# Optimization experiments

Hardware: AMD Instinct MI355X
Metric: run time of the kernel (lower is better)

The kernel has to match this reference:

```python
import jax, jax.numpy as jnp
import numpy as np

GAMMA = 2.5
K = 4
RHO = 0.085
TAU_CLIP = 5.0
NUM_HEADS = 8


def setup_inputs() -> dict:
    key = jax.random.key(0)
    ks = jax.random.split(key, 4)
    B, T, C = 2, 2048, 512
    x = jax.random.normal(ks[0], (B, T, C), jnp.float32)
    tau = jax.random.uniform(ks[1], (B, T, T), jnp.float32)
    s = 1.0 / np.sqrt(C)
    Wqkv = jax.random.normal(ks[2], (C, 3 * C), jnp.float32) * s
    bqkv = jnp.zeros((3 * C,), jnp.float32)
    Wproj = jax.random.normal(ks[3], (C, C), jnp.float32) * s
    bproj = jnp.zeros((C,), jnp.float32)
    return dict(x=x, tau=tau, Wqkv=Wqkv, bqkv=bqkv, Wproj=Wproj, bproj=bproj)


def reference(x, tau, Wqkv, bqkv, Wproj, bproj):
    B, T, C = x.shape
    H = NUM_HEADS
    D = C // H
    qkv = x @ Wqkv + bqkv                       # [B,T,3C]
    q, k, v = jnp.split(qkv, 3, axis=-1)
    q = q.reshape(B, T, H, D).transpose(0, 2, 1, 3)   # [B,H,T,D]
    k = k.reshape(B, T, H, D).transpose(0, 2, 1, 3)
    v = v.reshape(B, T, H, D).transpose(0, 2, 1, 3)
    scale = D ** -0.5
    logits = jnp.einsum('bhtd,bhsd->bhts', q, k) * scale   # [B,H,T,T]
    pheromone_bias = GAMMA * jnp.log(tau + 1e-8)           # [B,T,T]
    logits = logits + pheromone_bias[:, None]
    # top-K keys per query from tau define the sparse mask (LOCAL_WINDOW=0)
    k_val = min(K, T)
    idx = jax.lax.top_k(tau, k_val)[1]                     # [B,T,K]
    mask = jnp.zeros((B, T, T), bool).at[
        jnp.arange(B)[:, None, None], jnp.arange(T)[None, :, None], idx
    ].set(True)
    logits = jnp.where(mask[:, None], logits, -jnp.inf)
    attn = jax.nn.softmax(logits, axis=-1)                 # [B,H,T,T]
    # EMA pheromone (tau) update, no gradient in original (torch.no_grad)
    signal = attn.mean(axis=1)                             # [B,T,T]
    tau_new = (1.0 - RHO) * tau + signal ** 3
    tau_new = tau_new / (tau_new.sum(axis=-1, keepdims=True) + 1e-8)
    tau_new = jnp.minimum(tau_new, TAU_CLIP)
    tau_new = jax.lax.stop_gradient(tau_new)
    out = jnp.einsum('bhts,bhsd->bthd', attn, v).reshape(B, T, C)
    out = out @ Wproj + bproj
    return out, tau_new
```

## Files before the change

### kernel.cpp

```cpp
#include <hip/hip_runtime.h>
#include <hip/hip_bf16.h>
#include <math.h>

#define BB 2
#define TT 2048
#define CC 512
#define HH 8
#define DD 64
#define KK 4
#define C3 1536
#define MROWS (BB*TT)

#define G1_NT (C3/64)
#define G1_BLOCKS (G1_NT*(MROWS/128))
#define G2_NT (CC/64)
#define G2_BLOCKS (G2_NT*(MROWS/128))

typedef __attribute__((ext_vector_type(8))) short bf16x8;
typedef __attribute__((ext_vector_type(4))) float floatx4;

static __device__ __forceinline__ unsigned short f2bf(float f) {
  unsigned int u = __float_as_uint(f);
  return (unsigned short)((u + 0x7fffu + ((u >> 16) & 1u)) >> 16);
}
static __device__ __forceinline__ float bf2f(unsigned short u) {
  return __uint_as_float(((unsigned int)u) << 16);
}

template<bool BF16OUT>
static __device__ __forceinline__ void gemm_body(
    int bid, int nt,
    const unsigned short* __restrict__ A,
    const unsigned short* __restrict__ Bt,
    const float* __restrict__ bias,
    void* __restrict__ Cout, int N, int K) {
  __shared__ bf16x8 As[128 * 4];
  __shared__ bf16x8 Bs[64 * 4];
  const int tid  = threadIdx.x;
  const int wave = tid >> 6;
  const int lane = tid & 63;
  const int n0 = (bid % nt) * 64;
  const int m0 = (bid / nt) * 128;
  const int m_off = (wave >> 1) * 64;
  const int n_off = (wave & 1) * 32;
  const int lrow = lane >> 2;
  const int lx   = ((lane & 3) ^ ((lane >> 3) & 3)) * 8;
  const int fr = lane & 15;
  const int fq = lane >> 4;
  const int key = (fr >> 1) & 3;

  floatx4 acc[4][2];
#pragma unroll
  for (int i = 0; i < 4; ++i)
#pragma unroll
    for (int j = 0; j < 2; ++j) acc[i][j] = (floatx4){0.f, 0.f, 0.f, 0.f};

  for (int k0 = 0; k0 < K; k0 += 32) {
#pragma unroll
    for (int s = 0; s < 2; ++s) {
      int q = wave * 2 + s;
      const unsigned short* ga = A + (size_t)(m0 + q * 16 + lrow) * K + k0 + lx;
      __builtin_amdgcn_global_load_lds(
          (const __attribute__((address_space(1))) void*)ga,
          (__attribute__((address_space(3))) void*)((char*)As + q * 1024), 16, 0, 0);
    }
    const unsigned short* gb = Bt + (size_t)(n0 + wave * 16 + lrow) * K + k0 + lx;
    __builtin_amdgcn_global_load_lds(
        (const __attribute__((address_space(1))) void*)gb,
        (__attribute__((address_space(3))) void*)((char*)Bs + wave * 1024), 16, 0, 0);
    __syncthreads();
    bf16x8 a[4], b[2];
#pragma unroll
    for (int i = 0; i < 4; ++i)
      a[i] = As[(m_off + i * 16 + fr) * 4 + (fq ^ key)];
#pragma unroll
    for (int j = 0; j < 2; ++j)
      b[j] = Bs[(n_off + j * 16 + fr) * 4 + (fq ^ key)];
#pragma unroll
    for (int i = 0; i < 4; ++i)
#pragma unroll
      for (int j = 0; j < 2; ++j)
        acc[i][j] = __builtin_amdgcn_mfma_f32_16x16x32_bf16(a[i], b[j], acc[i][j], 0, 0, 0);
    __syncthreads();
  }
#pragma unroll
  for (int j = 0; j < 2; ++j) {
    int col = n0 + n_off + j * 16 + fr;
    float bv = bias[col];
#pragma unroll
    for (int i = 0; i < 4; ++i) {
#pragma unroll
      for (int r = 0; r < 4; ++r) {
        int row = m0 + m_off + i * 16 + fq * 4 + r;
        float v = acc[i][j][r] + bv;
        if (BF16OUT) ((unsigned short*)Cout)[(size_t)row * N + col] = f2bf(v);
        else         ((float*)Cout)[(size_t)row * N + col] = v;
      }
    }
  }
}

static __device__ __forceinline__ bool kv_better(float av, int ai, float bv, int bi) {
  return av > bv || (av == bv && ai < bi);
}
static __device__ __forceinline__ void kv_ce(float* v, int* i, int a, int b) {
  if (!kv_better(v[a], i[a], v[b], i[b])) {
    float tv = v[a]; v[a] = v[b]; v[b] = tv;
    int   ti = i[a]; i[a] = i[b]; i[b] = ti;
  }
}
static __device__ __forceinline__ void kv_merge(
    float* av, int* ai, const float* bv, const int* bi) {
  float cv[4]; int ci[4];
#pragma unroll
  for (int j = 0; j < 4; ++j) {
    bool t = kv_better(av[j], ai[j], bv[3 - j], bi[3 - j]);
    cv[j] = t ? av[j] : bv[3 - j];
    ci[j] = t ? ai[j] : bi[3 - j];
  }
  kv_ce(cv, ci, 0, 2); kv_ce(cv, ci, 1, 3);
  kv_ce(cv, ci, 0, 1); kv_ce(cv, ci, 2, 3);
#pragma unroll
  for (int j = 0; j < 4; ++j) { av[j] = cv[j]; ai[j] = ci[j]; }
}

static __device__ __forceinline__ void transpose_body(
    int t, int nbx, const float* __restrict__ W, unsigned short* __restrict__ Wt,
    int R, int Cn) {
  __shared__ unsigned short tile[32][33];
  const int c0 = (t % nbx) * 32, r0 = (t / nbx) * 32;
  const int tx = threadIdx.x & 31, ty = threadIdx.x >> 5;
#pragma unroll
  for (int i = 0; i < 4; ++i) {
    int r = ty + i * 8;
    tile[r][tx] = f2bf(W[(size_t)(r0 + r) * Cn + c0 + tx]);
  }
  __syncthreads();
#pragma unroll
  for (int i = 0; i < 4; ++i) {
    int r = ty + i * 8;
    Wt[(size_t)(c0 + r) * R + r0 + tx] = tile[tx][r];
  }
}

__global__ __launch_bounds__(256) void prep_kernel(
    const float* __restrict__ x, unsigned short* __restrict__ x_bf,
    const float* __restrict__ Wqkv, unsigned short* __restrict__ wqkv_t,
    const float* __restrict__ Wproj, unsigned short* __restrict__ wproj_t) {
  const int bid = blockIdx.x;
  if (bid < 1024) {
    int g = bid * 256 + threadIdx.x;
    const float4* p = (const float4*)x;
    float4 f0 = p[g * 2], f1 = p[g * 2 + 1];
    union { unsigned short u[8]; uint4 v; } pk;
    pk.u[0]=f2bf(f0.x); pk.u[1]=f2bf(f0.y); pk.u[2]=f2bf(f0.z); pk.u[3]=f2bf(f0.w);
    pk.u[4]=f2bf(f1.x); pk.u[5]=f2bf(f1.y); pk.u[6]=f2bf(f1.z); pk.u[7]=f2bf(f1.w);
    ((uint4*)x_bf)[g] = pk.v;
  } else if (bid < 1024 + 768) {
    transpose_body(bid - 1024, C3 / 32, Wqkv, wqkv_t, CC, C3);
  } else {
    transpose_body(bid - 1792, CC / 32, Wproj, wproj_t, CC, CC);
  }
}

__global__ __launch_bounds__(256) void gemm1_kernel(
    const unsigned short* __restrict__ x_bf,
    const unsigned short* __restrict__ wqkv_t,
    const float* __restrict__ bqkv, unsigned short* __restrict__ qkv_bf) {
  gemm_body<true>(blockIdx.x, G1_NT, x_bf, wqkv_t, bqkv, qkv_bf, C3, CC);
}

__global__ __launch_bounds__(256) void row_kernel(
    const unsigned short* __restrict__ qkv, const float* __restrict__ tau,
    unsigned short* __restrict__ attn_bf, float* __restrict__ tau_out) {
  const int row  = blockIdx.x;
  const int b    = row >> 11;
  const int tid  = threadIdx.x;
  const int wv   = tid >> 6;
  const int lane = tid & 63;

  __shared__ int   idx4[KK];
  __shared__ float tau4[KK];
  __shared__ float ps[HH][KK];
  __shared__ float s3s[KK];
  __shared__ float swv[4][4];
  __shared__ int   swi[4][4];
  __shared__ float wsum[4];
  __shared__ float tot;

  const float4* rp = (const float4*)(tau + (size_t)row * TT);
  float4 f0 = rp[tid * 2], f1 = rp[tid * 2 + 1];
  float e[8] = { f0.x, f0.y, f0.z, f0.w, f1.x, f1.y, f1.z, f1.w };
  const int base = tid * 8;

  float tv[4] = { -1e30f, -1e30f, -1e30f, -1e30f };
  int   ti[4] = { 1 << 30, 1 << 30, 1 << 30, 1 << 30 };
#pragma unroll
  for (int k = 0; k < 8; ++k) {
    float v = e[k];
    if (v > tv[3]) {
      tv[3] = v; ti[3] = base + k;
      if (tv[3] > tv[2]) { float a=tv[2]; tv[2]=tv[3]; tv[3]=a; int c=ti[2]; ti[2]=ti[3]; ti[3]=c; }
      if (tv[2] > tv[1]) { float a=tv[1]; tv[1]=tv[2]; tv[2]=a; int c=ti[1]; ti[1]=ti[2]; ti[2]=c; }
      if (tv[1] > tv[0]) { float a=tv[0]; tv[0]=tv[1]; tv[1]=a; int c=ti[0]; ti[0]=ti[1]; ti[1]=c; }
    }
  }
#pragma unroll
  for (int step = 1; step <= 32; step <<= 1) {
    float bv[4]; int bi[4];
#pragma unroll
    for (int j = 0; j < 4; ++j) {
      bv[j] = __shfl_xor(tv[j], step, 64);
      bi[j] = __shfl_xor(ti[j], step, 64);
    }
    kv_merge(tv, ti, bv, bi);
  }
  if (lane == 0) {
#pragma unroll
    for (int j = 0; j < 4; ++j) { swv[wv][j] = tv[j]; swi[wv][j] = ti[j]; }
  }
  __syncthreads();
  if (tid == 0) {
    float m0[4], m1[4]; int x0[4], x1[4];
#pragma unroll
    for (int j = 0; j < 4; ++j) { m0[j] = swv[0][j]; x0[j] = swi[0][j]; }
#pragma unroll
    for (int j = 0; j < 4; ++j) { m1[j] = swv[1][j]; x1[j] = swi[1][j]; }
    kv_merge(m0, x0, m1, x1);
#pragma unroll
    for (int j = 0; j < 4; ++j) { m1[j] = swv[2][j]; x1[j] = swi[2][j]; }
    float m2[4]; int x2[4];
#pragma unroll
    for (int j = 0; j < 4; ++j) { m2[j] = swv[3][j]; x2[j] = swi[3][j]; }
    kv_merge(m1, x1, m2, x2);
    kv_merge(m0, x0, m1, x1);
#pragma unroll
    for (int j = 0; j < 4; ++j) { idx4[j] = x0[j]; tau4[j] = m0[j]; }
  }
  __syncthreads();

  int   i4[KK]; float t4[KK];
#pragma unroll
  for (int j = 0; j < KK; ++j) { i4[j] = idx4[j]; t4[j] = tau4[j]; }

#pragma unroll
  for (int hh = 0; hh < 2; ++hh) {
    const int h = wv + hh * 4;
    const float q = bf2f(qkv[(size_t)row * C3 + h * DD + lane]);
    float kv[KK], vv[KK];
#pragma unroll
    for (int j = 0; j < KK; ++j) {
      size_t bs = ((size_t)(b * TT + i4[j])) * C3 + h * DD + lane;
      kv[j] = bf2f(qkv[bs + CC]);
      vv[j] = bf2f(qkv[bs + 2 * CC]);
    }
    float p[KK];
#pragma unroll
    for (int j = 0; j < KK; ++j) p[j] = q * kv[j];
#pragma unroll
    for (int off = 32; off > 0; off >>= 1)
#pragma unroll
      for (int j = 0; j < KK; ++j) p[j] += __shfl_xor(p[j], off, 64);
    float logit[KK];
#pragma unroll
    for (int j = 0; j < KK; ++j)
      logit[j] = p[j] * 0.125f + 2.5f * logf(t4[j] + 1e-8f);
    float m = fmaxf(fmaxf(logit[0], logit[1]), fmaxf(logit[2], logit[3]));
    float den = 0.f;
#pragma unroll
    for (int j = 0; j < KK; ++j) { p[j] = expf(logit[j] - m); den += p[j]; }
    float inv = 1.f / den;
#pragma unroll
    for (int j = 0; j < KK; ++j) p[j] *= inv;
    float o = 0.f;
#pragma unroll
    for (int j = 0; j < KK; ++j) o += p[j] * vv[j];
    attn_bf[(size_t)row * CC + h * DD + lane] = f2bf(o);
    if (lane < KK) ps[h][lane] = p[lane];
  }
  __syncthreads();
  if (tid < KK) {
    float s = 0.f;
#pragma unroll
    for (int k = 0; k < HH; ++k) s += ps[k][tid];
    s *= (1.0f / HH);
    s3s[tid] = s * s * s;
  }
  __syncthreads();

  float s3[KK];
#pragma unroll
  for (int j = 0; j < KK; ++j) s3[j] = s3s[j];
  const float keep = 1.0f - 0.085f;
  float local = 0.f;
#pragma unroll
  for (int i = 0; i < 8; ++i) {
    float t = keep * e[i];
#pragma unroll
    for (int j = 0; j < KK; ++j)
      if (base + i == i4[j]) t += s3[j];
    e[i] = t;
    local += t;
  }
#pragma unroll
  for (int off = 32; off > 0; off >>= 1) local += __shfl_xor(local, off, 64);
  if (lane == 0) wsum[wv] = local;
  __syncthreads();
  if (tid == 0) tot = wsum[0] + wsum[1] + wsum[2] + wsum[3];
  __syncthreads();
  float inv = 1.f / (tot + 1e-8f);
  float4* op = (float4*)(tau_out + (size_t)row * TT);
  float4 o0 = { fminf(e[0]*inv,5.f), fminf(e[1]*inv,5.f), fminf(e[2]*inv,5.f), fminf(e[3]*inv,5.f) };
  float4 o1 = { fminf(e[4]*inv,5.f), fminf(e[5]*inv,5.f), fminf(e[6]*inv,5.f), fminf(e[7]*inv,5.f) };
  op[tid * 2] = o0;
  op[tid * 2 + 1] = o1;
}

__global__ __launch_bounds__(256) void gemm2_kernel(
    const unsigned short* __restrict__ attn_bf,
    const unsigned short* __restrict__ wproj_t,
    const float* __restrict__ bproj, float* __restrict__ out) {
  gemm_body<false>(blockIdx.x, G2_NT, attn_bf, wproj_t, bproj, out, CC, CC);
}

extern "C" void kernel_launch(void* const* d_in, const int* in_sizes, int n_in,
                              void* d_out, int out_size, void* d_ws, size_t ws_size,
                              hipStream_t stream) {
  const float* x     = (const float*)d_in[0];
  const float* tau   = (const float*)d_in[1];
  const float* Wqkv  = (const float*)d_in[2];
  const float* bqkv  = (const float*)d_in[3];
  const float* Wproj = (const float*)d_in[4];
  const float* bproj = (const float*)d_in[5];

  float* out     = (float*)d_out;
  float* tau_new = out + (size_t)MROWS * CC;

  char* w = (char*)d_ws;
  unsigned short* qkv_bf  = (unsigned short*)w; w += (size_t)MROWS * C3 * 2;
  unsigned short* x_bf    = (unsigned short*)w; w += (size_t)MROWS * CC * 2;
  unsigned short* wqkv_t  = (unsigned short*)w; w += (size_t)C3 * CC * 2;
  unsigned short* wproj_t = (unsigned short*)w; w += (size_t)CC * CC * 2;
  unsigned short* attn_bf = (unsigned short*)w;

  prep_kernel<<<2048, 256, 0, stream>>>(x, x_bf, Wqkv, wqkv_t, Wproj, wproj_t);

  gemm1_kernel<<<G1_BLOCKS, 256, 0, stream>>>(x_bf, wqkv_t, bqkv, qkv_bf);

  row_kernel<<<MROWS, 256, 0, stream>>>(qkv_bf, tau, attn_bf, tau_new);

  gemm2_kernel<<<G2_BLOCKS, 256, 0, stream>>>(attn_bf, wproj_t, bproj, out);
}
```

Measured before the change: 146.5 us.

## Add XCD-aware block swizzle, smaller gemm2 tiles, and early q load in row kernel

Remaps block IDs so consecutive tiles land on the same XCD for better L2 reuse in both GEMMs. Adds a 64x64-tile GEMM variant for the projection GEMM, doubling its block count to fill more CUs, at the cost of lower per-block data reuse. In the row kernel, the query loads are hoisted so they overlap with the top-k selection over tau.

```diff
diff --git a/kernel.cpp b/kernel.cpp
--- a/kernel.cpp
+++ b/kernel.cpp
@@ -14,7 +14,7 @@
 #define G1_NT (C3/64)
 #define G1_BLOCKS (G1_NT*(MROWS/128))
 #define G2_NT (CC/64)
-#define G2_BLOCKS (G2_NT*(MROWS/128))
+#define G2_BLOCKS (G2_NT*(MROWS/64))
 
 typedef __attribute__((ext_vector_type(8))) short bf16x8;
 typedef __attribute__((ext_vector_type(4))) float floatx4;
@@ -25,6 +25,11 @@
 }
 static __device__ __forceinline__ float bf2f(unsigned short u) {
   return __uint_as_float(((unsigned int)u) << 16);
+}
+
+static __device__ __forceinline__ int xcd_swz(int bid, int nblk) {
+  const int cpx = nblk >> 3;
+  return (bid & 7) * cpx + (bid >> 3);
 }
 
 template<bool BF16OUT>
@@ -100,6 +105,72 @@
   }
 }
 
+static __device__ __forceinline__ void gemm_body64(
+    int bid, int nt,
+    const unsigned short* __restrict__ A,
+    const unsigned short* __restrict__ Bt,
+    const float* __restrict__ bias,
+    float* __restrict__ Cout, int N, int K) {
+  __shared__ bf16x8 As[64 * 4];
+  __shared__ bf16x8 Bs[64 * 4];
+  const int tid  = threadIdx.x;
+  const int wave = tid >> 6;
+  const int lane = tid & 63;
+  const int n0 = (bid % nt) * 64;
+  const int m0 = (bid / nt) * 64;
+  const int m_off = (wave >> 1) * 32;
+  const int n_off = (wave & 1) * 32;
+  const int lrow = lane >> 2;
+  const int lx   = ((lane & 3) ^ ((lane >> 3) & 3)) * 8;
+  const int fr = lane & 15;
+  const int fq = lane >> 4;
+  const int key = (fr >> 1) & 3;
+
+  floatx4 acc[2][2];
+#pragma unroll
+  for (int i = 0; i < 2; ++i)
+#pragma unroll
+    for (int j = 0; j < 2; ++j) acc[i][j] = (floatx4){0.f, 0.f, 0.f, 0.f};
+
+  for (int k0 = 0; k0 < K; k0 += 32) {
+    const unsigned short* ga = A + (size_t)(m0 + wave * 16 + lrow) * K + k0 + lx;
+    __builtin_amdgcn_global_load_lds(
+        (const __attribute__((address_space(1))) void*)ga,
+        (__attribute__((address_space(3))) void*)((char*)As + wave * 1024), 16, 0, 0);
+    const unsigned short* gb = Bt + (size_t)(n0 + wave * 16 + lrow) * K + k0 + lx;
+    __builtin_amdgcn_global_load_lds(
+        (const __attribute__((address_space(1))) void*)gb,
+        (__attribute__((address_space(3))) void*)((char*)Bs + wave * 1024), 16, 0, 0);
+    __syncthreads();
+    bf16x8 a[2], b[2];
+#pragma unroll
+    for (int i = 0; i < 2; ++i)
+      a[i] = As[(m_off + i * 16 + fr) * 4 + (fq ^ key)];
+#pragma unroll
+    for (int j = 0; j < 2; ++j)
+      b[j] = Bs[(n_off + j * 16 + fr) * 4 + (fq ^ key)];
+#pragma unroll
+    for (int i = 0; i < 2; ++i)
+#pragma unroll
+      for (int j = 0; j < 2; ++j)
+        acc[i][j] = __builtin_amdgcn_mfma_f32_16x16x32_bf16(a[i], b[j], acc[i][j], 0, 0, 0);
+    __syncthreads();
+  }
+#pragma unroll
+  for (int j = 0; j < 2; ++j) {
+    int col = n0 + n_off + j * 16 + fr;
+    float bv = bias[col];
+#pragma unroll
+    for (int i = 0; i < 2; ++i) {
+#pragma unroll
+      for (int r = 0; r < 4; ++r) {
+        int row = m0 + m_off + i * 16 + fq * 4 + r;
+        Cout[(size_t)row * N + col] = acc[i][j][r] + bv;
+      }
+    }
+  }
+}
+
 static __device__ __forceinline__ bool kv_better(float av, int ai, float bv, int bi) {
   return av > bv || (av == bv && ai < bi);
 }
@@ -167,7 +238,8 @@
     const unsigned short* __restrict__ x_bf,
     const unsigned short* __restrict__ wqkv_t,
     const float* __restrict__ bqkv, unsigned short* __restrict__ qkv_bf) {
-  gemm_body<true>(blockIdx.x, G1_NT, x_bf, wqkv_t, bqkv, qkv_bf, C3, CC);
+  gemm_body<true>(xcd_swz(blockIdx.x, G1_BLOCKS), G1_NT,
+                  x_bf, wqkv_t, bqkv, qkv_bf, C3, CC);
 }
 
 __global__ __launch_bounds__(256) void row_kernel(
@@ -190,6 +262,9 @@
 
   const float4* rp = (const float4*)(tau + (size_t)row * TT);
   float4 f0 = rp[tid * 2], f1 = rp[tid * 2 + 1];
+  float qv[2];
+  qv[0] = bf2f(qkv[(size_t)row * C3 + wv * DD + lane]);
+  qv[1] = bf2f(qkv[(size_t)row * C3 + (wv + 4) * DD + lane]);
   float e[8] = { f0.x, f0.y, f0.z, f0.w, f1.x, f1.y, f1.z, f1.w };
   const int base = tid * 8;
 
@@ -246,7 +321,7 @@
 #pragma unroll
   for (int hh = 0; hh < 2; ++hh) {
     const int h = wv + hh * 4;
-    const float q = bf2f(qkv[(size_t)row * C3 + h * DD + lane]);
+    const float q = qv[hh];
     float kv[KK], vv[KK];
 #pragma unroll
     for (int j = 0; j < KK; ++j) {
@@ -320,7 +395,8 @@
     const unsigned short* __restrict__ attn_bf,
     const unsigned short* __restrict__ wproj_t,
     const float* __restrict__ bproj, float* __restrict__ out) {
-  gemm_body<false>(blockIdx.x, G2_NT, attn_bf, wproj_t, bproj, out, CC, CC);
+  gemm_body64(xcd_swz(blockIdx.x, G2_BLOCKS), G2_NT,
+              attn_bf, wproj_t, bproj, out, CC, CC);
 }
 
 extern "C" void kernel_launch(void* const* d_in, const int* in_sizes, int n_in,
```

Result: faster. 143.0 us (-2.4%).
